# Performance work log

Hardware: AMD Instinct MI355X
Metric: run time of the kernel (lower is better)

The kernel has to match this reference:

```python
import jax, jax.numpy as jnp
import numpy as np

B, LQ, LK, H = 4, 256, 512, 256

def setup_inputs() -> dict:
    key = jax.random.key(0)
    ks = jax.random.split(key, 9)
    return {
        "query": jax.random.normal(ks[0], (B, LQ, H), dtype=jnp.float32),
        "key": jax.random.normal(ks[1], (B, LK, H), dtype=jnp.float32),
        "value": jax.random.normal(ks[2], (B, LK, H), dtype=jnp.float32),
        "mask": jax.random.randint(ks[3], (B, LK), 0, 2, dtype=jnp.int32),
        "Wq": jax.random.normal(ks[4], (H, H), dtype=jnp.float32) / np.sqrt(H),
        "bq": jnp.zeros((H,), dtype=jnp.float32),
        "Wk": jax.random.normal(ks[5], (H, H), dtype=jnp.float32) / np.sqrt(H),
        "bk": jnp.zeros((H,), dtype=jnp.float32),
        "v": jax.random.normal(ks[6], (H,), dtype=jnp.float32) / np.sqrt(H),
        "bv": jnp.zeros((), dtype=jnp.float32),
    }

def reference(query, key, value, mask, Wq, bq, Wk, bk, v, bv):
    # Linear projections: y = x @ W^T + b (torch nn.Linear convention)
    q = query @ Wq.T + bq            # [B, Lq, H]
    k = key @ Wk.T + bk              # [B, Lk, H]
    # Broadcast add -> tanh -> project to scalar with v
    s = jnp.tanh(q[:, :, None, :] + k[:, None, :, :])   # [B, Lq, Lk, H]
    scores = jnp.einsum('bqkh,h->bqk', s, v) + bv        # [B, Lq, Lk]
    scores = jnp.where(mask[:, None, :] == 0, -jnp.inf, scores)
    attn_weights = jax.nn.softmax(scores, axis=-1)       # [B, Lq, Lk]
    attn_output = jnp.einsum('bqk,bkh->bqh', attn_weights, value)
    return (attn_output, attn_weights)
```

## Files before the change

kernel.cpp:

```cpp
#include <hip/hip_runtime.h>
#include <math.h>

#define NB  4
#define NLQ 256
#define NLK 512
#define NH  256

#define SCALE_2LOG2E 2.885390081777927f
#define LOG2E        1.4426950408889634f

__global__ __launch_bounds__(256) void setup_kernel(
    const float* __restrict__ Wq, const float* __restrict__ Wk,
    const int* __restrict__ mask,
    float* __restrict__ Wtq, float* __restrict__ Wtk,
    int* __restrict__ act, int* __restrict__ nact)
{
    const int blk = blockIdx.x;
    const int t   = threadIdx.x;

    if (blk < 32) {
        __shared__ float ts[64][65];
        const int m    = blk >> 4;
        const int tile = blk & 15;
        const int h0 = (tile >> 2) * 64;
        const int c0 = (tile & 3) * 64;
        const float* W  = m ? Wk  : Wq;
        float*       Wt = m ? Wtk : Wtq;
        const int lr = t >> 4, lc = t & 15;
        #pragma unroll
        for (int i = 0; i < 4; ++i) {
            const int r = lr + 16 * i;
            const float4 d = *(const float4*)(W + (size_t)(h0 + r) * NH + c0 + lc * 4);
            ts[r][lc * 4 + 0] = d.x;
            ts[r][lc * 4 + 1] = d.y;
            ts[r][lc * 4 + 2] = d.z;
            ts[r][lc * 4 + 3] = d.w;
        }
        __syncthreads();
        #pragma unroll
        for (int i = 0; i < 4; ++i) {
            const int c = lr + 16 * i;
            float4 d;
            d.x = ts[lc * 4 + 0][c];
            d.y = ts[lc * 4 + 1][c];
            d.z = ts[lc * 4 + 2][c];
            d.w = ts[lc * 4 + 3][c];
            *(float4*)(Wt + (size_t)(c0 + c) * NH + h0 + lc * 4) = d;
        }
    } else if (blk < 32 + NB) {
        const int b = blk - 32;
        __shared__ int wcnt[8], wpre[9];
        const int lane = t & 63, wave = t >> 6;
        const int k1 = t, k2 = t + 256;
        const int m1 = mask[b * NLK + k1];
        const int m2 = mask[b * NLK + k2];
        const unsigned long long below = (1ULL << lane) - 1ULL;
        const unsigned long long bal1 = __ballot(m1 != 0);
        const unsigned long long bal2 = __ballot(m2 != 0);
        const int r1 = __popcll(bal1 & below);
        const int r2 = __popcll(bal2 & below);
        if (lane == 0) { wcnt[wave] = __popcll(bal1); wcnt[4 + wave] = __popcll(bal2); }
        __syncthreads();
        if (t == 0) {
            int s = 0;
            #pragma unroll
            for (int w = 0; w < 8; ++w) { wpre[w] = s; s += wcnt[w]; }
            wpre[8] = s;
        }
        __syncthreads();
        const int na = wpre[8];
        if (m1) act[b * NLK + wpre[wave]     + r1] = k1;
        if (m2) act[b * NLK + wpre[4 + wave] + r2] = k2;
        if (k1 >= na) act[b * NLK + k1] = 0;
        if (k2 >= na) act[b * NLK + k2] = 0;
        if (t == 0) nact[b] = na;
    }
}

__global__ __launch_bounds__(256) void prep_kernel(
    const float* __restrict__ query, const float* __restrict__ key,
    const float* __restrict__ Wtq, const float* __restrict__ bq,
    const float* __restrict__ Wtk, const float* __restrict__ bk,
    const int* __restrict__ act, const int* __restrict__ nact,
    float* __restrict__ qp, float* __restrict__ kp_ct)
{
    const int blk  = blockIdx.x;
    const int t    = threadIdx.x;
    const int wave = t >> 6;
    const int lane = t & 63;

    __shared__ float  xs[4][NH];
    __shared__ float4 ps[4][4][64];
    __shared__ int    ridx[4];

    const float *Wt, *bias;
    int b = 0, j0 = 0, r0 = 0, na = 0;
    const bool isq = (blk < NB * NLQ / 4);

    if (isq) {
        b  = blk & 3;
        r0 = b * NLQ + (blk >> 2) * 4;
        ((float4*)&xs[0][0])[t] = ((const float4*)(query + (size_t)r0 * NH))[t];
        Wt = Wtq; bias = bq;
    } else {
        const int idx = blk - 256;
        b  = idx & 3;
        j0 = (idx >> 2) * 4;
        na = nact[b];
        if (j0 >= na) return;
        if (t < 4) ridx[t] = act[b * NLK + ((j0 + t < na) ? (j0 + t) : j0)];
        __syncthreads();
        const int r = t >> 6, c4 = t & 63;
        ((float4*)xs[r])[c4] =
            ((const float4*)(key + ((size_t)b * NLK + ridx[r]) * NH))[c4];
        Wt = Wtk; bias = bk;
    }
    __syncthreads();

    float4 acc[4];
    #pragma unroll
    for (int r = 0; r < 4; ++r) acc[r] = (float4){0.f, 0.f, 0.f, 0.f};

    const int cbase = wave * 64;
    #pragma unroll 4
    for (int cc = 0; cc < 64; ++cc) {
        const int c = cbase + cc;
        const float4 w = *(const float4*)(Wt + (size_t)c * NH + lane * 4);
        #pragma unroll
        for (int r = 0; r < 4; ++r) {
            const float xv = xs[r][c];
            acc[r].x = fmaf(xv, w.x, acc[r].x);
            acc[r].y = fmaf(xv, w.y, acc[r].y);
            acc[r].z = fmaf(xv, w.z, acc[r].z);
            acc[r].w = fmaf(xv, w.w, acc[r].w);
        }
    }
    #pragma unroll
    for (int r = 0; r < 4; ++r) ps[wave][r][lane] = acc[r];
    __syncthreads();

    const int r = wave, l = lane;
    const float4 p0 = ps[0][r][l], p1 = ps[1][r][l];
    const float4 p2 = ps[2][r][l], p3 = ps[3][r][l];
    const float4 bb = *(const float4*)(bias + l * 4);
    float4 o;
    o.x = (p0.x + p1.x + p2.x + p3.x + bb.x) * SCALE_2LOG2E;
    o.y = (p0.y + p1.y + p2.y + p3.y + bb.y) * SCALE_2LOG2E;
    o.z = (p0.z + p1.z + p2.z + p3.z + bb.z) * SCALE_2LOG2E;
    o.w = (p0.w + p1.w + p2.w + p3.w + bb.w) * SCALE_2LOG2E;
    o.x = __builtin_amdgcn_exp2f(o.x);
    o.y = __builtin_amdgcn_exp2f(o.y);
    o.z = __builtin_amdgcn_exp2f(o.z);
    o.w = __builtin_amdgcn_exp2f(o.w);

    if (isq) {
        *(float4*)(qp + (size_t)(r0 + r) * NH + l * 4) = o;
    } else if (j0 + r < na) {
        const int j = j0 + r;
        kp_ct[((size_t)b * NH + l * 4 + 0) * NLK + j] = o.x;
        kp_ct[((size_t)b * NH + l * 4 + 1) * NLK + j] = o.y;
        kp_ct[((size_t)b * NH + l * 4 + 2) * NLK + j] = o.z;
        kp_ct[((size_t)b * NH + l * 4 + 3) * NLK + j] = o.w;
    }
}

__global__ __launch_bounds__(512) void attn_kernel(
    const float* __restrict__ qp, const float* __restrict__ kp_ct,
    const float* __restrict__ value, const int* __restrict__ mask,
    const int* __restrict__ act, const int* __restrict__ nact,
    const float* __restrict__ vvec,
    float* __restrict__ out_o, float* __restrict__ out_w)
{
    __shared__ float sc[4][NLK];
    __shared__ int   actl[NLK];
    __shared__ float eqs[4][NH];
    __shared__ float vvs[NH];
    __shared__ float4 buf4[4096];

    const int blk  = blockIdx.x;
    const int b    = blk & 3;
    const int q0   = (blk >> 2) * 4;
    const int t    = threadIdx.x;
    const int lane = t & 63;
    const int wave = t >> 6;

    const int na = nact[b];
    actl[t] = (t < na) ? act[b * NLK + t] : 0;
    if (t < NH) {
        eqs[0][t] = qp[(size_t)(b * NLQ + q0 + 0) * NH + t];
        eqs[1][t] = qp[(size_t)(b * NLQ + q0 + 1) * NH + t];
        eqs[2][t] = qp[(size_t)(b * NLQ + q0 + 2) * NH + t];
        eqs[3][t] = qp[(size_t)(b * NLQ + q0 + 3) * NH + t];
        vvs[t]    = vvec[t];
    }

    float* wrow = out_w + (size_t)(b * NLQ + q0) * NLK;
    if (!mask[b * NLK + t]) {
        wrow[t] = 0.f; wrow[NLK + t] = 0.f;
        wrow[2 * NLK + t] = 0.f; wrow[3 * NLK + t] = 0.f;
    }
    __syncthreads();

    const int cb = wave * 32;
    const float* kb  = kp_ct + ((size_t)b * NH + cb) * NLK;
    const float* eq0 = &eqs[0][cb];
    const float* eq1 = &eqs[1][cb];
    const float* eq2 = &eqs[2][cb];
    const float* eq3 = &eqs[3][cb];
    const float* vv  = &vvs[cb];

    float4 a0h0 = {0,0,0,0}, a1h0 = {0,0,0,0}, a2h0 = {0,0,0,0}, a3h0 = {0,0,0,0};
    float4 a0h1 = {0,0,0,0}, a1h1 = {0,0,0,0}, a2h1 = {0,0,0,0}, a3h1 = {0,0,0,0};
    if (na > 256) {
        #pragma unroll 4
        for (int c = 0; c < 32; ++c) {
            const float4 k1 = *(const float4*)(kb + (size_t)c * NLK + 4 * lane);
            const float4 k2 = *(const float4*)(kb + (size_t)c * NLK + 256 + 4 * lane);
            const float e0 = eq0[c], e1 = eq1[c], e2 = eq2[c], e3 = eq3[c];
            const float vh = vv[c];
            a0h0.x = fmaf(vh, __builtin_amdgcn_rcpf(fmaf(e0, k1.x, 1.f)), a0h0.x);
            a0h0.y = fmaf(vh, __builtin_amdgcn_rcpf(fmaf(e0, k1.y, 1.f)), a0h0.y);
            a0h0.z = fmaf(vh, __builtin_amdgcn_rcpf(fmaf(e0, k1.z, 1.f)), a0h0.z);
            a0h0.w = fmaf(vh, __builtin_amdgcn_rcpf(fmaf(e0, k1.w, 1.f)), a0h0.w);
            a1h0.x = fmaf(vh, __builtin_amdgcn_rcpf(fmaf(e1, k1.x, 1.f)), a1h0.x);
            a1h0.y = fmaf(vh, __builtin_amdgcn_rcpf(fmaf(e1, k1.y, 1.f)), a1h0.y);
            a1h0.z = fmaf(vh, __builtin_amdgcn_rcpf(fmaf(e1, k1.z, 1.f)), a1h0.z);
            a1h0.w = fmaf(vh, __builtin_amdgcn_rcpf(fmaf(e1, k1.w, 1.f)), a1h0.w);
            a2h0.x = fmaf(vh, __builtin_amdgcn_rcpf(fmaf(e2, k1.x, 1.f)), a2h0.x);
            a2h0.y = fmaf(vh, __builtin_amdgcn_rcpf(fmaf(e2, k1.y, 1.f)), a2h0.y);
            a2h0.z = fmaf(vh, __builtin_amdgcn_rcpf(fmaf(e2, k1.z, 1.f)), a2h0.z);
            a2h0.w = fmaf(vh, __builtin_amdgcn_rcpf(fmaf(e2, k1.w, 1.f)), a2h0.w);
            a3h0.x = fmaf(vh, __builtin_amdgcn_rcpf(fmaf(e3, k1.x, 1.f)), a3h0.x);
            a3h0.y = fmaf(vh, __builtin_amdgcn_rcpf(fmaf(e3, k1.y, 1.f)), a3h0.y);
            a3h0.z = fmaf(vh, __builtin_amdgcn_rcpf(fmaf(e3, k1.z, 1.f)), a3h0.z);
            a3h0.w = fmaf(vh, __builtin_amdgcn_rcpf(fmaf(e3, k1.w, 1.f)), a3h0.w);
            a0h1.x = fmaf(vh, __builtin_amdgcn_rcpf(fmaf(e0, k2.x, 1.f)), a0h1.x);
            a0h1.y = fmaf(vh, __builtin_amdgcn_rcpf(fmaf(e0, k2.y, 1.f)), a0h1.y);
            a0h1.z = fmaf(vh, __builtin_amdgcn_rcpf(fmaf(e0, k2.z, 1.f)), a0h1.z);
            a0h1.w = fmaf(vh, __builtin_amdgcn_rcpf(fmaf(e0, k2.w, 1.f)), a0h1.w);
            a1h1.x = fmaf(vh, __builtin_amdgcn_rcpf(fmaf(e1, k2.x, 1.f)), a1h1.x);
            a1h1.y = fmaf(vh, __builtin_amdgcn_rcpf(fmaf(e1, k2.y, 1.f)), a1h1.y);
            a1h1.z = fmaf(vh, __builtin_amdgcn_rcpf(fmaf(e1, k2.z, 1.f)), a1h1.z);
            a1h1.w = fmaf(vh, __builtin_amdgcn_rcpf(fmaf(e1, k2.w, 1.f)), a1h1.w);
            a2h1.x = fmaf(vh, __builtin_amdgcn_rcpf(fmaf(e2, k2.x, 1.f)), a2h1.x);
            a2h1.y = fmaf(vh, __builtin_amdgcn_rcpf(fmaf(e2, k2.y, 1.f)), a2h1.y);
            a2h1.z = fmaf(vh, __builtin_amdgcn_rcpf(fmaf(e2, k2.z, 1.f)), a2h1.z);
            a2h1.w = fmaf(vh, __builtin_amdgcn_rcpf(fmaf(e2, k2.w, 1.f)), a2h1.w);
            a3h1.x = fmaf(vh, __builtin_amdgcn_rcpf(fmaf(e3, k2.x, 1.f)), a3h1.x);
            a3h1.y = fmaf(vh, __builtin_amdgcn_rcpf(fmaf(e3, k2.y, 1.f)), a3h1.y);
            a3h1.z = fmaf(vh, __builtin_amdgcn_rcpf(fmaf(e3, k2.z, 1.f)), a3h1.z);
            a3h1.w = fmaf(vh, __builtin_amdgcn_rcpf(fmaf(e3, k2.w, 1.f)), a3h1.w);
        }
    } else {
        #pragma unroll 4
        for (int c = 0; c < 32; ++c) {
            const float4 k1 = *(const float4*)(kb + (size_t)c * NLK + 4 * lane);
            const float e0 = eq0[c], e1 = eq1[c], e2 = eq2[c], e3 = eq3[c];
            const float vh = vv[c];
            a0h0.x = fmaf(vh, __builtin_amdgcn_rcpf(fmaf(e0, k1.x, 1.f)), a0h0.x);
            a0h0.y = fmaf(vh, __builtin_amdgcn_rcpf(fmaf(e0, k1.y, 1.f)), a0h0.y);
            a0h0.z = fmaf(vh, __builtin_amdgcn_rcpf(fmaf(e0, k1.z, 1.f)), a0h0.z);
            a0h0.w = fmaf(vh, __builtin_amdgcn_rcpf(fmaf(e0, k1.w, 1.f)), a0h0.w);
            a1h0.x = fmaf(vh, __builtin_amdgcn_rcpf(fmaf(e1, k1.x, 1.f)), a1h0.x);
            a1h0.y = fmaf(vh, __builtin_amdgcn_rcpf(fmaf(e1, k1.y, 1.f)), a1h0.y);
            a1h0.z = fmaf(vh, __builtin_amdgcn_rcpf(fmaf(e1, k1.z, 1.f)), a1h0.z);
            a1h0.w = fmaf(vh, __builtin_amdgcn_rcpf(fmaf(e1, k1.w, 1.f)), a1h0.w);
            a2h0.x = fmaf(vh, __builtin_amdgcn_rcpf(fmaf(e2, k1.x, 1.f)), a2h0.x);
            a2h0.y = fmaf(vh, __builtin_amdgcn_rcpf(fmaf(e2, k1.y, 1.f)), a2h0.y);
            a2h0.z = fmaf(vh, __builtin_amdgcn_rcpf(fmaf(e2, k1.z, 1.f)), a2h0.z);
            a2h0.w = fmaf(vh, __builtin_amdgcn_rcpf(fmaf(e2, k1.w, 1.f)), a2h0.w);
            a3h0.x = fmaf(vh, __builtin_amdgcn_rcpf(fmaf(e3, k1.x, 1.f)), a3h0.x);
            a3h0.y = fmaf(vh, __builtin_amdgcn_rcpf(fmaf(e3, k1.y, 1.f)), a3h0.y);
            a3h0.z = fmaf(vh, __builtin_amdgcn_rcpf(fmaf(e3, k1.z, 1.f)), a3h0.z);
            a3h0.w = fmaf(vh, __builtin_amdgcn_rcpf(fmaf(e3, k1.w, 1.f)), a3h0.w);
        }
    }
    buf4[(0 * 8 + wave) * 128 + lane]      = a0h0;
    buf4[(0 * 8 + wave) * 128 + 64 + lane] = a0h1;
    buf4[(1 * 8 + wave) * 128 + lane]      = a1h0;
    buf4[(1 * 8 + wave) * 128 + 64 + lane] = a1h1;
    buf4[(2 * 8 + wave) * 128 + lane]      = a2h0;
    buf4[(2 * 8 + wave) * 128 + 64 + lane] = a2h1;
    buf4[(3 * 8 + wave) * 128 + lane]      = a3h0;
    buf4[(3 * 8 + wave) * 128 + 64 + lane] = a3h1;
    __syncthreads();
    {
        const float* pf = (const float*)buf4;
        #pragma unroll
        for (int r = 0; r < 4; ++r) {
            float s = 0.f;
            #pragma unroll
            for (int o = 0; o < 8; ++o)
                s += pf[(r * 8 + o) * 512 + t];
            sc[r][t] = (t < na) ? -2.f * s : -INFINITY;
        }
    }
    __syncthreads();

    if (wave < 4) {
        float* row = sc[wave];
        float vals[8];
        float m = -INFINITY;
        #pragma unroll
        for (int j8 = 0; j8 < 8; ++j8) {
            vals[j8] = row[lane + j8 * 64];
            m = fmaxf(m, vals[j8]);
        }
        #pragma unroll
        for (int s = 32; s >= 1; s >>= 1)
            m = fmaxf(m, __shfl_xor(m, s, 64));
        float sum = 0.0f;
        #pragma unroll
        for (int j8 = 0; j8 < 8; ++j8) {
            vals[j8] = __builtin_amdgcn_exp2f((vals[j8] - m) * LOG2E);
            sum += vals[j8];
        }
        #pragma unroll
        for (int s = 32; s >= 1; s >>= 1)
            sum += __shfl_xor(sum, s, 64);
        const float inv = __builtin_amdgcn_rcpf(sum);
        float* wout = out_w + (size_t)(b * NLQ + q0 + wave) * NLK;
        #pragma unroll
        for (int j8 = 0; j8 < 8; ++j8) {
            const int jj = lane + j8 * 64;
            const float w = vals[j8] * inv;
            row[jj] = w;
            if (jj < na) wout[actl[jj]] = w;
        }
    }
    __syncthreads();

    {
        const int c4 = lane * 4;
        const float* vb = value + (size_t)b * NLK * NH + c4;
        float4 o0 = {0,0,0,0}, o1 = {0,0,0,0}, o2 = {0,0,0,0}, o3 = {0,0,0,0};
        #pragma unroll 4
        for (int j = wave; j < na; j += 8) {
            const float w0 = sc[0][j];
            const float w1 = sc[1][j];
            const float w2 = sc[2][j];
            const float w3 = sc[3][j];
            const int   rj = actl[j];
            const float4 v4 = *(const float4*)(vb + (size_t)rj * NH);
            o0.x = fmaf(w0, v4.x, o0.x); o0.y = fmaf(w0, v4.y, o0.y);
            o0.z = fmaf(w0, v4.z, o0.z); o0.w = fmaf(w0, v4.w, o0.w);
            o1.x = fmaf(w1, v4.x, o1.x); o1.y = fmaf(w1, v4.y, o1.y);
            o1.z = fmaf(w1, v4.z, o1.z); o1.w = fmaf(w1, v4.w, o1.w);
            o2.x = fmaf(w2, v4.x, o2.x); o2.y = fmaf(w2, v4.y, o2.y);
            o2.z = fmaf(w2, v4.z, o2.z); o2.w = fmaf(w2, v4.w, o2.w);
            o3.x = fmaf(w3, v4.x, o3.x); o3.y = fmaf(w3, v4.y, o3.y);
            o3.z = fmaf(w3, v4.z, o3.z); o3.w = fmaf(w3, v4.w, o3.w);
        }
        __syncthreads();
        buf4[0 * 512 + t] = o0;
        buf4[1 * 512 + t] = o1;
        buf4[2 * 512 + t] = o2;
        buf4[3 * 512 + t] = o3;
        __syncthreads();
        if (t < 256) {
            const int row = t >> 6;
            const int l   = t & 63;
            float4 o = buf4[row * 512 + l];
            #pragma unroll
            for (int w = 1; w < 8; ++w) {
                const float4 s = buf4[row * 512 + l + 64 * w];
                o.x += s.x; o.y += s.y; o.z += s.z; o.w += s.w;
            }
            *(float4*)(out_o + (size_t)(b * NLQ + q0 + row) * NH + l * 4) = o;
        }
    }
}

extern "C" void kernel_launch(void* const* d_in, const int* in_sizes, int n_in,
                              void* d_out, int out_size, void* d_ws, size_t ws_size,
                              hipStream_t stream) {
    const float* query = (const float*)d_in[0];
    const float* key   = (const float*)d_in[1];
    const float* value = (const float*)d_in[2];
    const int*   mask  = (const int*)  d_in[3];
    const float* Wq    = (const float*)d_in[4];
    const float* bq    = (const float*)d_in[5];
    const float* Wk    = (const float*)d_in[6];
    const float* bk    = (const float*)d_in[7];
    const float* v     = (const float*)d_in[8];

    float* out_o = (float*)d_out;
    float* out_w = out_o + NB * NLQ * NH;

    float* qp    = (float*)d_ws;
    float* kp_ct = qp + NB * NLQ * NH;
    int*   act   = (int*)(kp_ct + NB * NH * NLK);
    int*   nact  = act + NB * NLK;

    const size_t base = (size_t)(NB * NLQ * NH) + (size_t)(NB * NH * NLK)
                      + NB * NLK + NB;
    float* wtq;
    if (ws_size >= (base + 2 * NH * NH) * sizeof(float)) {
        wtq = (float*)d_ws + base;
    } else {
        wtq = out_w + (size_t)NB * NLQ * NLK - 2 * NH * NH;
    }
    float* wtk = wtq + NH * NH;

    setup_kernel<<<36, 256, 0, stream>>>(Wq, Wk, mask, wtq, wtk, act, nact);
    prep_kernel<<<NB * NLQ / 4 + NB * NLK / 4, 256, 0, stream>>>(
        query, key, wtq, bq, wtk, bk, act, nact, qp, kp_ct);
    attn_kernel<<<NB * NLQ / 4, 512, 0, stream>>>(
        qp, kp_ct, value, mask, act, nact, v, out_o, out_w);
}
```

Before: 110.3 us.

## Double attention block to 1024 threads, splitting score and PV work across 16 waves

Launches the attention kernel with 1024 threads and splits the additive-score loop across 16 waves: by sequence half for long active sets, by finer H chunks for short ones. The final PV accumulation is strided over 16 waves. The aim is more waves per CU and fewer live accumulators per thread, hiding latency in the rcp-heavy score loop. The cost is larger cross-wave reductions through shared memory, plus extra barrier participants.

```diff
diff --git a/kernel.cpp b/kernel.cpp
--- a/kernel.cpp
+++ b/kernel.cpp
@@ -164,7 +164,7 @@
     }
 }
 
-__global__ __launch_bounds__(512) void attn_kernel(
+__global__ __launch_bounds__(1024) void attn_kernel(
     const float* __restrict__ qp, const float* __restrict__ kp_ct,
     const float* __restrict__ value, const int* __restrict__ mask,
     const int* __restrict__ act, const int* __restrict__ nact,
@@ -185,7 +185,7 @@
     const int wave = t >> 6;
 
     const int na = nact[b];
-    actl[t] = (t < na) ? act[b * NLK + t] : 0;
+    if (t < NLK) actl[t] = (t < na) ? act[b * NLK + t] : 0;
     if (t < NH) {
         eqs[0][t] = qp[(size_t)(b * NLQ + q0 + 0) * NH + t];
         eqs[1][t] = qp[(size_t)(b * NLQ + q0 + 1) * NH + t];
@@ -194,106 +194,113 @@
         vvs[t]    = vvec[t];
     }
 
-    float* wrow = out_w + (size_t)(b * NLQ + q0) * NLK;
-    if (!mask[b * NLK + t]) {
-        wrow[t] = 0.f; wrow[NLK + t] = 0.f;
-        wrow[2 * NLK + t] = 0.f; wrow[3 * NLK + t] = 0.f;
-    }
-    __syncthreads();
-
-    const int cb = wave * 32;
-    const float* kb  = kp_ct + ((size_t)b * NH + cb) * NLK;
-    const float* eq0 = &eqs[0][cb];
-    const float* eq1 = &eqs[1][cb];
-    const float* eq2 = &eqs[2][cb];
-    const float* eq3 = &eqs[3][cb];
-    const float* vv  = &vvs[cb];
-
-    float4 a0h0 = {0,0,0,0}, a1h0 = {0,0,0,0}, a2h0 = {0,0,0,0}, a3h0 = {0,0,0,0};
-    float4 a0h1 = {0,0,0,0}, a1h1 = {0,0,0,0}, a2h1 = {0,0,0,0}, a3h1 = {0,0,0,0};
+    if (t < NLK) {
+        float* wrow = out_w + (size_t)(b * NLQ + q0) * NLK;
+        if (!mask[b * NLK + t]) {
+            wrow[t] = 0.f; wrow[NLK + t] = 0.f;
+            wrow[2 * NLK + t] = 0.f; wrow[3 * NLK + t] = 0.f;
+        }
+    }
+    __syncthreads();
+
     if (na > 256) {
+        const int oct  = wave & 7;
+        const int half = wave >> 3;
+        const int cb   = oct * 32;
+        const int s0   = half * 256 + 4 * lane;
+        const float* kb  = kp_ct + ((size_t)b * NH + cb) * NLK;
+        const float* eq0 = &eqs[0][cb];
+        const float* eq1 = &eqs[1][cb];
+        const float* eq2 = &eqs[2][cb];
+        const float* eq3 = &eqs[3][cb];
+        const float* vv  = &vvs[cb];
+        float4 a0 = {0,0,0,0}, a1 = {0,0,0,0}, a2 = {0,0,0,0}, a3 = {0,0,0,0};
         #pragma unroll 4
         for (int c = 0; c < 32; ++c) {
-            const float4 k1 = *(const float4*)(kb + (size_t)c * NLK + 4 * lane);
-            const float4 k2 = *(const float4*)(kb + (size_t)c * NLK + 256 + 4 * lane);
+            const float4 k1 = *(const float4*)(kb + (size_t)c * NLK + s0);
             const float e0 = eq0[c], e1 = eq1[c], e2 = eq2[c], e3 = eq3[c];
             const float vh = vv[c];
-            a0h0.x = fmaf(vh, __builtin_amdgcn_rcpf(fmaf(e0, k1.x, 1.f)), a0h0.x);
-            a0h0.y = fmaf(vh, __builtin_amdgcn_rcpf(fmaf(e0, k1.y, 1.f)), a0h0.y);
-            a0h0.z = fmaf(vh, __builtin_amdgcn_rcpf(fmaf(e0, k1.z, 1.f)), a0h0.z);
-            a0h0.w = fmaf(vh, __builtin_amdgcn_rcpf(fmaf(e0, k1.w, 1.f)), a0h0.w);
-            a1h0.x = fmaf(vh, __builtin_amdgcn_rcpf(fmaf(e1, k1.x, 1.f)), a1h0.x);
-            a1h0.y = fmaf(vh, __builtin_amdgcn_rcpf(fmaf(e1, k1.y, 1.f)), a1h0.y);
-            a1h0.z = fmaf(vh, __builtin_amdgcn_rcpf(fmaf(e1, k1.z, 1.f)), a1h0.z);
-            a1h0.w = fmaf(vh, __builtin_amdgcn_rcpf(fmaf(e1, k1.w, 1.f)), a1h0.w);
-            a2h0.x = fmaf(vh, __builtin_amdgcn_rcpf(fmaf(e2, k1.x, 1.f)), a2h0.x);
-            a2h0.y = fmaf(vh, __builtin_amdgcn_rcpf(fmaf(e2, k1.y, 1.f)), a2h0.y);
-            a2h0.z = fmaf(vh, __builtin_amdgcn_rcpf(fmaf(e2, k1.z, 1.f)), a2h0.z);
-            a2h0.w = fmaf(vh, __builtin_amdgcn_rcpf(fmaf(e2, k1.w, 1.f)), a2h0.w);
-            a3h0.x = fmaf(vh, __builtin_amdgcn_rcpf(fmaf(e3, k1.x, 1.f)), a3h0.x);
-            a3h0.y = fmaf(vh, __builtin_amdgcn_rcpf(fmaf(e3, k1.y, 1.f)), a3h0.y);
-            a3h0.z = fmaf(vh, __builtin_amdgcn_rcpf(fmaf(e3, k1.z, 1.f)), a3h0.z);
-            a3h0.w = fmaf(vh, __builtin_amdgcn_rcpf(fmaf(e3, k1.w, 1.f)), a3h0.w);
-            a0h1.x = fmaf(vh, __builtin_amdgcn_rcpf(fmaf(e0, k2.x, 1.f)), a0h1.x);
-            a0h1.y = fmaf(vh, __builtin_amdgcn_rcpf(fmaf(e0, k2.y, 1.f)), a0h1.y);
-            a0h1.z = fmaf(vh, __builtin_amdgcn_rcpf(fmaf(e0, k2.z, 1.f)), a0h1.z);
-            a0h1.w = fmaf(vh, __builtin_amdgcn_rcpf(fmaf(e0, k2.w, 1.f)), a0h1.w);
-            a1h1.x = fmaf(vh, __builtin_amdgcn_rcpf(fmaf(e1, k2.x, 1.f)), a1h1.x);
-            a1h1.y = fmaf(vh, __builtin_amdgcn_rcpf(fmaf(e1, k2.y, 1.f)), a1h1.y);
-            a1h1.z = fmaf(vh, __builtin_amdgcn_rcpf(fmaf(e1, k2.z, 1.f)), a1h1.z);
-            a1h1.w = fmaf(vh, __builtin_amdgcn_rcpf(fmaf(e1, k2.w, 1.f)), a1h1.w);
-            a2h1.x = fmaf(vh, __builtin_amdgcn_rcpf(fmaf(e2, k2.x, 1.f)), a2h1.x);
-            a2h1.y = fmaf(vh, __builtin_amdgcn_rcpf(fmaf(e2, k2.y, 1.f)), a2h1.y);
-            a2h1.z = fmaf(vh, __builtin_amdgcn_rcpf(fmaf(e2, k2.z, 1.f)), a2h1.z);
-            a2h1.w = fmaf(vh, __builtin_amdgcn_rcpf(fmaf(e2, k2.w, 1.f)), a2h1.w);
-            a3h1.x = fmaf(vh, __builtin_amdgcn_rcpf(fmaf(e3, k2.x, 1.f)), a3h1.x);
-            a3h1.y = fmaf(vh, __builtin_amdgcn_rcpf(fmaf(e3, k2.y, 1.f)), a3h1.y);
-            a3h1.z = fmaf(vh, __builtin_amdgcn_rcpf(fmaf(e3, k2.z, 1.f)), a3h1.z);
-            a3h1.w = fmaf(vh, __builtin_amdgcn_rcpf(fmaf(e3, k2.w, 1.f)), a3h1.w);
-        }
+            a0.x = fmaf(vh, __builtin_amdgcn_rcpf(fmaf(e0, k1.x, 1.f)), a0.x);
+            a0.y = fmaf(vh, __builtin_amdgcn_rcpf(fmaf(e0, k1.y, 1.f)), a0.y);
+            a0.z = fmaf(vh, __builtin_amdgcn_rcpf(fmaf(e0, k1.z, 1.f)), a0.z);
+            a0.w = fmaf(vh, __builtin_amdgcn_rcpf(fmaf(e0, k1.w, 1.f)), a0.w);
+            a1.x = fmaf(vh, __builtin_amdgcn_rcpf(fmaf(e1, k1.x, 1.f)), a1.x);
+            a1.y = fmaf(vh, __builtin_amdgcn_rcpf(fmaf(e1, k1.y, 1.f)), a1.y);
+            a1.z = fmaf(vh, __builtin_amdgcn_rcpf(fmaf(e1, k1.z, 1.f)), a1.z);
+            a1.w = fmaf(vh, __builtin_amdgcn_rcpf(fmaf(e1, k1.w, 1.f)), a1.w);
+            a2.x = fmaf(vh, __builtin_amdgcn_rcpf(fmaf(e2, k1.x, 1.f)), a2.x);
+            a2.y = fmaf(vh, __builtin_amdgcn_rcpf(fmaf(e2, k1.y, 1.f)), a2.y);
+            a2.z = fmaf(vh, __builtin_amdgcn_rcpf(fmaf(e2, k1.z, 1.f)), a2.z);
+            a2.w = fmaf(vh, __builtin_amdgcn_rcpf(fmaf(e2, k1.w, 1.f)), a2.w);
+            a3.x = fmaf(vh, __builtin_amdgcn_rcpf(fmaf(e3, k1.x, 1.f)), a3.x);
+            a3.y = fmaf(vh, __builtin_amdgcn_rcpf(fmaf(e3, k1.y, 1.f)), a3.y);
+            a3.z = fmaf(vh, __builtin_amdgcn_rcpf(fmaf(e3, k1.z, 1.f)), a3.z);
+            a3.w = fmaf(vh, __builtin_amdgcn_rcpf(fmaf(e3, k1.w, 1.f)), a3.w);
+        }
+        buf4[(0 * 8 + oct) * 128 + half * 64 + lane] = a0;
+        buf4[(1 * 8 + oct) * 128 + half * 64 + lane] = a1;
+        buf4[(2 * 8 + oct) * 128 + half * 64 + lane] = a2;
+        buf4[(3 * 8 + oct) * 128 + half * 64 + lane] = a3;
     } else {
+        const int cb = wave * 16;
+        const int s0 = 4 * lane;
+        const float* kb  = kp_ct + ((size_t)b * NH + cb) * NLK;
+        const float* eq0 = &eqs[0][cb];
+        const float* eq1 = &eqs[1][cb];
+        const float* eq2 = &eqs[2][cb];
+        const float* eq3 = &eqs[3][cb];
+        const float* vv  = &vvs[cb];
+        float4 a0 = {0,0,0,0}, a1 = {0,0,0,0}, a2 = {0,0,0,0}, a3 = {0,0,0,0};
         #pragma unroll 4
-        for (int c = 0; c < 32; ++c) {
-            const float4 k1 = *(const float4*)(kb + (size_t)c * NLK + 4 * lane);
+        for (int c = 0; c < 16; ++c) {
+            const float4 k1 = *(const float4*)(kb + (size_t)c * NLK + s0);
             const float e0 = eq0[c], e1 = eq1[c], e2 = eq2[c], e3 = eq3[c];
             const float vh = vv[c];
-            a0h0.x = fmaf(vh, __builtin_amdgcn_rcpf(fmaf(e0, k1.x, 1.f)), a0h0.x);
-            a0h0.y = fmaf(vh, __builtin_amdgcn_rcpf(fmaf(e0, k1.y, 1.f)), a0h0.y);
-            a0h0.z = fmaf(vh, __builtin_amdgcn_rcpf(fmaf(e0, k1.z, 1.f)), a0h0.z);
-            a0h0.w = fmaf(vh, __builtin_amdgcn_rcpf(fmaf(e0, k1.w, 1.f)), a0h0.w);
-            a1h0.x = fmaf(vh, __builtin_amdgcn_rcpf(fmaf(e1, k1.x, 1.f)), a1h0.x);
-            a1h0.y = fmaf(vh, __builtin_amdgcn_rcpf(fmaf(e1, k1.y, 1.f)), a1h0.y);
-            a1h0.z = fmaf(vh, __builtin_amdgcn_rcpf(fmaf(e1, k1.z, 1.f)), a1h0.z);
-            a1h0.w = fmaf(vh, __builtin_amdgcn_rcpf(fmaf(e1, k1.w, 1.f)), a1h0.w);
-            a2h0.x = fmaf(vh, __builtin_amdgcn_rcpf(fmaf(e2, k1.x, 1.f)), a2h0.x);
-            a2h0.y = fmaf(vh, __builtin_amdgcn_rcpf(fmaf(e2, k1.y, 1.f)), a2h0.y);
-            a2h0.z = fmaf(vh, __builtin_amdgcn_rcpf(fmaf(e2, k1.z, 1.f)), a2h0.z);
-            a2h0.w = fmaf(vh, __builtin_amdgcn_rcpf(fmaf(e2, k1.w, 1.f)), a2h0.w);
-            a3h0.x = fmaf(vh, __builtin_amdgcn_rcpf(fmaf(e3, k1.x, 1.f)), a3h0.x);
-            a3h0.y = fmaf(vh, __builtin_amdgcn_rcpf(fmaf(e3, k1.y, 1.f)), a3h0.y);
-            a3h0.z = fmaf(vh, __builtin_amdgcn_rcpf(fmaf(e3, k1.z, 1.f)), a3h0.z);
-            a3h0.w = fmaf(vh, __builtin_amdgcn_rcpf(fmaf(e3, k1.w, 1.f)), a3h0.w);
-        }
-    }
-    buf4[(0 * 8 + wave) * 128 + lane]      = a0h0;
-    buf4[(0 * 8 + wave) * 128 + 64 + lane] = a0h1;
-    buf4[(1 * 8 + wave) * 128 + lane]      = a1h0;
-    buf4[(1 * 8 + wave) * 128 + 64 + lane] = a1h1;
-    buf4[(2 * 8 + wave) * 128 + lane]      = a2h0;
-    buf4[(2 * 8 + wave) * 128 + 64 + lane] = a2h1;
-    buf4[(3 * 8 + wave) * 128 + lane]      = a3h0;
-    buf4[(3 * 8 + wave) * 128 + 64 + lane] = a3h1;
-    __syncthreads();
-    {
+            a0.x = fmaf(vh, __builtin_amdgcn_rcpf(fmaf(e0, k1.x, 1.f)), a0.x);
+            a0.y = fmaf(vh, __builtin_amdgcn_rcpf(fmaf(e0, k1.y, 1.f)), a0.y);
+            a0.z = fmaf(vh, __builtin_amdgcn_rcpf(fmaf(e0, k1.z, 1.f)), a0.z);
+            a0.w = fmaf(vh, __builtin_amdgcn_rcpf(fmaf(e0, k1.w, 1.f)), a0.w);
+            a1.x = fmaf(vh, __builtin_amdgcn_rcpf(fmaf(e1, k1.x, 1.f)), a1.x);
+            a1.y = fmaf(vh, __builtin_amdgcn_rcpf(fmaf(e1, k1.y, 1.f)), a1.y);
+            a1.z = fmaf(vh, __builtin_amdgcn_rcpf(fmaf(e1, k1.z, 1.f)), a1.z);
+            a1.w = fmaf(vh, __builtin_amdgcn_rcpf(fmaf(e1, k1.w, 1.f)), a1.w);
+            a2.x = fmaf(vh, __builtin_amdgcn_rcpf(fmaf(e2, k1.x, 1.f)), a2.x);
+            a2.y = fmaf(vh, __builtin_amdgcn_rcpf(fmaf(e2, k1.y, 1.f)), a2.y);
+            a2.z = fmaf(vh, __builtin_amdgcn_rcpf(fmaf(e2, k1.z, 1.f)), a2.z);
+            a2.w = fmaf(vh, __builtin_amdgcn_rcpf(fmaf(e2, k1.w, 1.f)), a2.w);
+            a3.x = fmaf(vh, __builtin_amdgcn_rcpf(fmaf(e3, k1.x, 1.f)), a3.x);
+            a3.y = fmaf(vh, __builtin_amdgcn_rcpf(fmaf(e3, k1.y, 1.f)), a3.y);
+            a3.z = fmaf(vh, __builtin_amdgcn_rcpf(fmaf(e3, k1.z, 1.f)), a3.z);
+            a3.w = fmaf(vh, __builtin_amdgcn_rcpf(fmaf(e3, k1.w, 1.f)), a3.w);
+        }
+        buf4[(0 * 16 + wave) * 64 + lane] = a0;
+        buf4[(1 * 16 + wave) * 64 + lane] = a1;
+        buf4[(2 * 16 + wave) * 64 + lane] = a2;
+        buf4[(3 * 16 + wave) * 64 + lane] = a3;
+    }
+    __syncthreads();
+
+    if (na > 256) {
+        const int s  = t & 511;
+        const int rb = (t >> 9) * 2;
         const float* pf = (const float*)buf4;
         #pragma unroll
-        for (int r = 0; r < 4; ++r) {
-            float s = 0.f;
+        for (int ri = 0; ri < 2; ++ri) {
+            const int r = rb + ri;
+            float sum = 0.f;
             #pragma unroll
-            for (int o = 0; o < 8; ++o)
-                s += pf[(r * 8 + o) * 512 + t];
-            sc[r][t] = (t < na) ? -2.f * s : -INFINITY;
-        }
+            for (int o = 0; o < 8; ++o) sum += pf[(r * 8 + o) * 512 + s];
+            sc[r][s] = (s < na) ? -2.f * sum : -INFINITY;
+        }
+    } else {
+        const int s = t & 255;
+        const int r = t >> 8;
+        const float* pf = (const float*)buf4;
+        float sum = 0.f;
+        #pragma unroll
+        for (int o = 0; o < 16; ++o) sum += pf[(r * 16 + o) * 256 + s];
+        sc[r][s]       = (s < na) ? -2.f * sum : -INFINITY;
+        sc[r][s + 256] = -INFINITY;
     }
     __syncthreads();
 
@@ -335,7 +342,7 @@
         const float* vb = value + (size_t)b * NLK * NH + c4;
         float4 o0 = {0,0,0,0}, o1 = {0,0,0,0}, o2 = {0,0,0,0}, o3 = {0,0,0,0};
         #pragma unroll 4
-        for (int j = wave; j < na; j += 8) {
+        for (int j = wave; j < na; j += 16) {
             const float w0 = sc[0][j];
             const float w1 = sc[1][j];
             const float w2 = sc[2][j];
@@ -352,18 +359,18 @@
             o3.z = fmaf(w3, v4.z, o3.z); o3.w = fmaf(w3, v4.w, o3.w);
         }
         __syncthreads();
-        buf4[0 * 512 + t] = o0;
-        buf4[1 * 512 + t] = o1;
-        buf4[2 * 512 + t] = o2;
-        buf4[3 * 512 + t] = o3;
+        buf4[0 * 1024 + t] = o0;
+        buf4[1 * 1024 + t] = o1;
+        buf4[2 * 1024 + t] = o2;
+        buf4[3 * 1024 + t] = o3;
         __syncthreads();
         if (t < 256) {
             const int row = t >> 6;
             const int l   = t & 63;
-            float4 o = buf4[row * 512 + l];
+            float4 o = buf4[row * 1024 + l];
             #pragma unroll
-            for (int w = 1; w < 8; ++w) {
-                const float4 s = buf4[row * 512 + l + 64 * w];
+            for (int w = 1; w < 16; ++w) {
+                const float4 s = buf4[row * 1024 + l + 64 * w];
                 o.x += s.x; o.y += s.y; o.z += s.z; o.w += s.w;
             }
             *(float4*)(out_o + (size_t)(b * NLQ + q0 + row) * NH + l * 4) = o;
@@ -405,6 +412,6 @@
     setup_kernel<<<36, 256, 0, stream>>>(Wq, Wk, mask, wtq, wtk, act, nact);
     prep_kernel<<<NB * NLQ / 4 + NB * NLK / 4, 256, 0, stream>>>(
         query, key, wtq, bq, wtk, bk, act, nact, qp, kp_ct);
-    attn_kernel<<<NB * NLQ / 4, 512, 0, stream>>>(
+    attn_kernel<<<NB * NLQ / 4, 1024, 0, stream>>>(
         qp, kp_ct, value, mask, act, nact, v, out_o, out_w);
 }
```

Result: faster. 108.1 us (-2.0%).
